# Kernel optimization log

Measured on AMD Instinct MI355X. Metric: run time of the kernel, lower is better.

Reference implementation:

```python
import jax, jax.numpy as jnp
import numpy as np

PAD = 2  # F.conv2d(padding=2) with 5x5 kernels -> SAME

def setup_inputs() -> dict:
    key = jax.random.key(0)
    k1, k2 = jax.random.split(key)
    B, H, W, C = 64, 128, 128, 3
    KH, KW, N = 5, 5, 10  # last_frames(2) * num_transformed_images(5)
    images = jax.random.uniform(k1, (B, H, W, C), dtype=jnp.float32)
    kernels = jax.random.uniform(k2, (B, KH, KW, N), dtype=jnp.float32)
    return {"images": images, "kernels": kernels}


def reference(images, kernels):
    """Faithful JAX version of apply_cdna_kernels.

    images:  [B, H, W, C]
    kernels: [B, KH, KW, N]
    returns: [N, B, C, H, W] (the torch code returns N split tensors of
             shape [1, B, C, H, W]; we return the equivalent stacked array).
    Implemented as a single grouped cross-correlation with
    feature_group_count=B, fusing the per-batch F.conv2d loop.
    """
    B, H, W, C = images.shape
    _, KH, KW, N = kernels.shape
    # torch: images.permute([3,0,1,2]) -> [C, B, H, W]; treat C as conv batch,
    # B as input channels, one input channel per group.
    inp = jnp.transpose(images, (3, 0, 1, 2))  # [C, B, H, W]
    # weights: group b owns output channels b*N:(b+1)*N, each 1 input channel
    w = jnp.transpose(kernels, (0, 3, 1, 2)).reshape(B * N, 1, KH, KW)
    out = jax.lax.conv_general_dilated(
        inp, w,
        window_strides=(1, 1),
        padding=((PAD, PAD), (PAD, PAD)),
        feature_group_count=B,
        dimension_numbers=("NCHW", "OIHW", "NCHW"),
    )  # [C, B*N, H, W]
    out = out.reshape(C, B, N, H, W)
    return jnp.transpose(out, (2, 1, 0, 3, 4))  # [N, B, C, H, W]
```

## Files before the change

kernel.cpp:

```cpp
#include <hip/hip_runtime.h>


#define B_  64
#define H_  128
#define W_  128
#define C_  3
#define N_  10
#define KH_ 5
#define KW_ 5
#define TH_ 8
#define TWB 64
#define HALO 2
#define LDS_ROW ((TWB + 2*HALO) * C_)
#define LDS_ELEMS ((TH_ + 2*HALO) * LDS_ROW)

__global__ __launch_bounds__(256, 4) void cdna_apply_kernel(
    const float* __restrict__ images,
    const float* __restrict__ kernels,
    float* __restrict__ out)
{
    __shared__ float s_img[LDS_ELEMS];

    const int tid = threadIdx.x;
    const int bid = blockIdx.x;
    const int b   = bid >> 5;
    const int t   = bid & 31;
    const int by  = t >> 1;
    const int bx  = t & 1;
    const int y0  = by * TH_;
    const int x0  = bx * TWB;

    const long img_base = (long)b * (H_ * W_ * C_);
    const int  colf0    = x0 * C_ - HALO * C_;
    #pragma unroll
    for (int k = 0; k < (LDS_ELEMS + 255) / 256; ++k) {
        int i = tid + k * 256;
        if (i < LDS_ELEMS) {
            int yy = i / LDS_ROW;
            int r  = i - yy * LDS_ROW;
            int y  = y0 + yy - HALO;
            int cf = colf0 + r;
            float v = 0.0f;
            if ((unsigned)y < (unsigned)H_ && (unsigned)cf < (unsigned)(W_ * C_))
                v = images[img_base + (long)y * (W_ * C_) + cf];
            s_img[i] = v;
        }
    }
    __syncthreads();

    const int tx = tid & 31;
    const int ty = tid >> 5;

    const float* __restrict__ kb = kernels + b * (KH_ * KW_ * N_);

    float acc0[N_ * C_];
    float acc1[N_ * C_];
    #pragma unroll
    for (int i = 0; i < N_ * C_; ++i) { acc0[i] = 0.0f; acc1[i] = 0.0f; }

    #pragma unroll 1
    for (int kh = 0; kh < KH_; ++kh) {
        const float* row = &s_img[(ty + kh) * LDS_ROW + 6 * tx];
        float p[(KW_ + 1) * C_];
        #pragma unroll
        for (int i = 0; i < (KW_ + 1) * C_; ++i) p[i] = row[i];

        const float* __restrict__ wrow = kb + kh * (KW_ * N_);
        #pragma unroll
        for (int kw = 0; kw < KW_; ++kw) {
            #pragma unroll
            for (int n = 0; n < N_; ++n) {
                const float wgt = wrow[kw * N_ + n];
                #pragma unroll
                for (int c = 0; c < C_; ++c) {
                    acc0[n * C_ + c] = fmaf(p[kw * C_ + c],       wgt, acc0[n * C_ + c]);
                    acc1[n * C_ + c] = fmaf(p[kw * C_ + C_ + c],  wgt, acc1[n * C_ + c]);
                }
            }
        }
    }

    const int h = y0 + ty;
    const int w = x0 + 2 * tx;
    float* ob = out + (long)b * (C_ * H_ * W_) + (long)h * W_ + w;
    #pragma unroll
    for (int n = 0; n < N_; ++n) {
        #pragma unroll
        for (int c = 0; c < C_; ++c) {
            float2 v;
            v.x = acc0[n * C_ + c];
            v.y = acc1[n * C_ + c];
            *(float2*)(ob + (long)n * ((long)B_ * C_ * H_ * W_) + (long)c * (H_ * W_)) = v;
        }
    }
}

extern "C" void kernel_launch(void* const* d_in, const int* in_sizes, int n_in,
                              void* d_out, int out_size, void* d_ws, size_t ws_size,
                              hipStream_t stream) {
    const float* images  = (const float*)d_in[0];
    const float* kernels = (const float*)d_in[1];
    float* out = (float*)d_out;

    const int grid = B_ * (H_ / TH_) * (W_ / TWB);
    cdna_apply_kernel<<<grid, 256, 0, stream>>>(images, kernels, out);
}
```

Before: 153.1 us.

## Store image tile channel-planar in LDS and use nontemporal output stores

Rearranges the shared-memory tile from interleaved HWC into per-channel planes with padded row pitch, so each thread reads contiguous 2-stride positions per channel and LDS bank conflicts from the 6-float stride drop. Output stores switch to nontemporal float2 builtins to avoid polluting cache with the large write-only result. This adds index division work in the load phase.

```diff
diff --git a/kernel.cpp b/kernel.cpp
--- a/kernel.cpp
+++ b/kernel.cpp
@@ -11,8 +11,14 @@
 #define TH_ 8
 #define TWB 64
 #define HALO 2
-#define LDS_ROW ((TWB + 2*HALO) * C_)
-#define LDS_ELEMS ((TH_ + 2*HALO) * LDS_ROW)
+#define TROWS (TH_ + 2*HALO)
+#define TCOLS (TWB + 2*HALO)
+#define PROW  70
+#define PLANE (TROWS * PROW)
+#define LDS_ELEMS (C_ * PLANE)
+#define GROW  (TCOLS * C_)
+
+typedef float f2_t __attribute__((ext_vector_type(2)));
 
 __global__ __launch_bounds__(256, 4) void cdna_apply_kernel(
     const float* __restrict__ images,
@@ -33,17 +39,19 @@
     const long img_base = (long)b * (H_ * W_ * C_);
     const int  colf0    = x0 * C_ - HALO * C_;
     #pragma unroll
-    for (int k = 0; k < (LDS_ELEMS + 255) / 256; ++k) {
-        int i = tid + k * 256;
-        if (i < LDS_ELEMS) {
-            int yy = i / LDS_ROW;
-            int r  = i - yy * LDS_ROW;
+    for (int k = 0; k < (TROWS * GROW + 255) / 256; ++k) {
+        int g = tid + k * 256;
+        if (g < TROWS * GROW) {
+            int yy = g / GROW;
+            int r  = g - yy * GROW;
+            int x  = r / C_;
+            int c  = r - x * C_;
             int y  = y0 + yy - HALO;
             int cf = colf0 + r;
             float v = 0.0f;
             if ((unsigned)y < (unsigned)H_ && (unsigned)cf < (unsigned)(W_ * C_))
                 v = images[img_base + (long)y * (W_ * C_) + cf];
-            s_img[i] = v;
+            s_img[c * PLANE + yy * PROW + x] = v;
         }
     }
     __syncthreads();
@@ -60,10 +68,13 @@
 
     #pragma unroll 1
     for (int kh = 0; kh < KH_; ++kh) {
-        const float* row = &s_img[(ty + kh) * LDS_ROW + 6 * tx];
-        float p[(KW_ + 1) * C_];
+        float p[C_][KW_ + 1];
         #pragma unroll
-        for (int i = 0; i < (KW_ + 1) * C_; ++i) p[i] = row[i];
+        for (int c = 0; c < C_; ++c) {
+            const float* row = &s_img[c * PLANE + (ty + kh) * PROW + 2 * tx];
+            #pragma unroll
+            for (int j = 0; j < KW_ + 1; ++j) p[c][j] = row[j];
+        }
 
         const float* __restrict__ wrow = kb + kh * (KW_ * N_);
         #pragma unroll
@@ -73,8 +84,8 @@
                 const float wgt = wrow[kw * N_ + n];
                 #pragma unroll
                 for (int c = 0; c < C_; ++c) {
-                    acc0[n * C_ + c] = fmaf(p[kw * C_ + c],       wgt, acc0[n * C_ + c]);
-                    acc1[n * C_ + c] = fmaf(p[kw * C_ + C_ + c],  wgt, acc1[n * C_ + c]);
+                    acc0[n * C_ + c] = fmaf(p[c][kw],     wgt, acc0[n * C_ + c]);
+                    acc1[n * C_ + c] = fmaf(p[c][kw + 1], wgt, acc1[n * C_ + c]);
                 }
             }
         }
@@ -87,10 +98,12 @@
     for (int n = 0; n < N_; ++n) {
         #pragma unroll
         for (int c = 0; c < C_; ++c) {
-            float2 v;
+            f2_t v;
             v.x = acc0[n * C_ + c];
             v.y = acc1[n * C_ + c];
-            *(float2*)(ob + (long)n * ((long)B_ * C_ * H_ * W_) + (long)c * (H_ * W_)) = v;
+            __builtin_nontemporal_store(
+                v, (f2_t*)(ob + (long)n * ((long)B_ * C_ * H_ * W_)
+                              + (long)c * (H_ * W_)));
         }
     }
 }
```

Result: no change. 154.3 us (+0.8%).
